# Kernel optimization log

Hardware: AMD Instinct MI355X
Metric: run time of the kernel (lower is better)

Reference implementation:

```python
import jax, jax.numpy as jnp
import numpy as np

N_EMBD = 2048
N_HEAD = 16
D_HEAD = N_EMBD // N_HEAD  # 128
B, T = 2, 2048
ROPE_BASE = 10000.0


def _rope_cos_sin(T, d, dtype):
    # (T, d) cos/sin tables, rotate-half convention
    inv_freq = 1.0 / (ROPE_BASE ** (jnp.arange(0, d, 2, dtype=jnp.float32) / d))
    ang = jnp.arange(T, dtype=jnp.float32)[:, None] * inv_freq[None, :]  # (T, d/2)
    cos = jnp.concatenate([jnp.cos(ang), jnp.cos(ang)], axis=-1).astype(dtype)
    sin = jnp.concatenate([jnp.sin(ang), jnp.sin(ang)], axis=-1).astype(dtype)
    return cos, sin


def _rotate_half(x):
    d = x.shape[-1] // 2
    return jnp.concatenate([-x[..., d:], x[..., :d]], axis=-1)


def setup_inputs() -> dict:
    key = jax.random.key(0)
    k1, k2, k3 = jax.random.split(key, 3)
    x = jax.random.normal(k1, (B, T, N_EMBD), dtype=jnp.float32)
    w_qkv = jax.random.normal(k2, (3 * N_EMBD, N_EMBD), dtype=jnp.float32) * 0.02
    w_proj = jax.random.normal(k3, (N_EMBD, N_EMBD), dtype=jnp.float32) * 0.02
    return {"x": x, "w_qkv": w_qkv, "w_proj": w_proj}


def reference(x, w_qkv, w_proj):
    Bq, Tq, C = x.shape
    H, D = N_HEAD, D_HEAD
    # fused QKV projection (torch Linear: x @ W.T)
    qkv = jnp.einsum('btc,fc->btf', x, w_qkv).reshape(Bq, Tq, 3, H, D)
    q, k, v = qkv[:, :, 0], qkv[:, :, 1], qkv[:, :, 2]  # (B,T,H,D)
    q = jnp.transpose(q, (0, 2, 1, 3))  # (B,H,T,D)
    k = jnp.transpose(k, (0, 2, 1, 3))
    v = jnp.transpose(v, (0, 2, 1, 3))
    # RoPE (start_pos = 0)
    cos, sin = _rope_cos_sin(Tq, D, x.dtype)  # (T,D)
    q = q * cos[None, None] + _rotate_half(q) * sin[None, None]
    k = k * cos[None, None] + _rotate_half(k) * sin[None, None]
    # causal SDPA
    scale = 1.0 / jnp.sqrt(jnp.asarray(D, x.dtype))
    scores = jnp.einsum('bhqd,bhkd->bhqk', q, k) * scale  # (B,H,T,T)
    causal = jnp.tril(jnp.ones((Tq, Tq), dtype=bool))
    scores = jnp.where(causal[None, None], scores, jnp.asarray(-jnp.inf, x.dtype))
    attn = jax.nn.softmax(scores, axis=-1)
    y = jnp.einsum('bhqk,bhkd->bhqd', attn, v)  # (B,H,T,D)
    y = jnp.transpose(y, (0, 2, 1, 3)).reshape(Bq, Tq, C)
    y = jnp.einsum('btc,fc->btf', y, w_proj)
    return y
```

## Files before the change

kernel.cpp:

```cpp
#include <hip/hip_runtime.h>
#include <hip/hip_bf16.h>
#include <math.h>

typedef __attribute__((ext_vector_type(8))) short short8;
typedef __attribute__((ext_vector_type(4))) short short4_t;
typedef __attribute__((ext_vector_type(4))) float f32x4;

#define Bb 2
#define Tt 2048
#define Hh 16
#define Dd 128
#define Cc 2048
#define Ff 6144

__device__ __forceinline__ size_t packed_idx(int row, int k) {
  return ((((size_t)(row >> 7) * 64 + (k >> 5)) * 8 + ((row >> 4) & 7)) * 512)
         + ((((k >> 3) & 3) * 16 + (row & 15)) * 8) + (k & 7);
}

__device__ __forceinline__ void gload_lds16(const void* g, void* l) {
  __builtin_amdgcn_global_load_lds(
      (const __attribute__((address_space(1))) void*)g,
      (__attribute__((address_space(3))) void*)l, 16, 0, 0);
}

__global__ __launch_bounds__(256) void pack_cast(
    const float* __restrict__ in, __hip_bfloat16* __restrict__ out, int n16)
{
  int t = blockIdx.x * 256 + threadIdx.x;
  if (t >= n16) return;
  int l = t & 63;
  int granule_lin = t >> 6;
  int g = granule_lin & 7;
  int slab = granule_lin >> 3;
  int ks = slab & 63;
  int m_tile = slab >> 6;
  int row = m_tile * 128 + g * 16 + (l & 15);
  int k = ks * 32 + (l >> 4) * 8;
  const float* src = in + (size_t)row * 2048 + k;
  float4 v0 = *(const float4*)src;
  float4 v1 = *(const float4*)(src + 4);
  __hip_bfloat16 tmp[8] = {
      __float2bfloat16(v0.x), __float2bfloat16(v0.y),
      __float2bfloat16(v0.z), __float2bfloat16(v0.w),
      __float2bfloat16(v1.x), __float2bfloat16(v1.y),
      __float2bfloat16(v1.z), __float2bfloat16(v1.w)};
  *(short8*)(out + (size_t)t * 8) = *(const short8*)tmp;
}

__device__ __forceinline__ void store_out(__hip_bfloat16* p, float v) { *p = __float2bfloat16(v); }
__device__ __forceinline__ void store_out(float* p, float v) { *p = v; }

template <typename OutT>
__global__ __launch_bounds__(512) void gemm_pk9(
    const __hip_bfloat16* __restrict__ Ap,
    const __hip_bfloat16* __restrict__ Bp,
    OutT* __restrict__ Cm, int N)
{
  __shared__ __align__(16) __hip_bfloat16 L[49152];
  const int tid  = threadIdx.x;
  const int wave = tid >> 6;
  const int lane = tid & 63;
  const int quad = lane >> 4;
  const int l16  = lane & 15;
  const int wm = wave >> 1;
  const int wn = wave & 1;
  const int bm = blockIdx.y * 256;
  const int bn = blockIdx.x * 128;
  const int NT = 32;
  const int ah = wm >> 1;
  const int ag = (wm & 1) * 4;

  const char* pA[2][2];
  const char* pB[2];
#pragma unroll
  for (int h = 0; h < 2; h++) {
#pragma unroll
    for (int c = 0; c < 2; c++) {
      int gi = wave * 2 + c;
      pA[h][c] = (const char*)Ap +
          ((size_t)(((bm >> 7) + h) * 64 + (gi >> 3)) * 8 + (gi & 7)) * 1024 + lane * 16;
    }
    pB[h] = (const char*)Bp +
        ((size_t)((bn >> 7) * 64 + h) * 8 + wave) * 1024 + lane * 16;
  }

#pragma unroll
  for (int h = 0; h < 2; h++) {
    gload_lds16(pA[h][0], &L[h * 12288 + (wave * 2 + 0) * 512]);
    gload_lds16(pA[h][1], &L[h * 12288 + (wave * 2 + 1) * 512]);
    gload_lds16(pB[h],    &L[h * 12288 + 8192 + wave * 512]);
    pA[h][0] += 16384; pA[h][1] += 16384; pB[h] += 16384;
  }

  f32x4 acc[4][4];
#pragma unroll
  for (int i = 0; i < 4; i++)
#pragma unroll
    for (int j = 0; j < 4; j++)
#pragma unroll
      for (int r = 0; r < 4; r++) acc[i][j][r] = 0.f;

#pragma unroll 1
  for (int t = 0; t < NT; ++t) {
    const int rs = (t & 1) * 2;
    const int ws = 2 - rs;
    const bool pre = (t + 1 < NT);

    if (pre) {
      gload_lds16(pA[0][0], &L[ws * 12288 + (wave * 2 + 0) * 512]);
      gload_lds16(pA[0][1], &L[ws * 12288 + (wave * 2 + 1) * 512]);
      gload_lds16(pB[0],    &L[ws * 12288 + 8192 + wave * 512]);
      __builtin_amdgcn_s_waitcnt(0xF73);
    } else {
      __builtin_amdgcn_s_waitcnt(0xF70);
    }
    __builtin_amdgcn_s_barrier();

    const __hip_bfloat16* A0 = &L[(rs + ah) * 12288];
    short8 bf[4][2];
#pragma unroll
    for (int j = 0; j < 4; j++)
#pragma unroll
      for (int k2 = 0; k2 < 2; k2++)
        bf[j][k2] = *(const short8*)(&L[(rs + k2) * 12288 + 8192 + (wn * 4 + j) * 512 + lane * 8]);
    {
      short8 af[2][2];
#pragma unroll
      for (int i = 0; i < 2; i++)
#pragma unroll
        for (int k2 = 0; k2 < 2; k2++)
          af[i][k2] = *(const short8*)(A0 + (k2 * 8 + ag + i) * 512 + lane * 8);
      __builtin_amdgcn_s_setprio(1);
#pragma unroll
      for (int i = 0; i < 2; i++)
#pragma unroll
        for (int j = 0; j < 4; j++)
#pragma unroll
          for (int k2 = 0; k2 < 2; k2++)
            acc[i][j] = __builtin_amdgcn_mfma_f32_16x16x32_bf16(
                af[i][k2], bf[j][k2], acc[i][j], 0, 0, 0);
      __builtin_amdgcn_s_setprio(0);
    }
    __builtin_amdgcn_s_barrier();

    if (pre) {
      gload_lds16(pA[1][0], &L[(ws + 1) * 12288 + (wave * 2 + 0) * 512]);
      gload_lds16(pA[1][1], &L[(ws + 1) * 12288 + (wave * 2 + 1) * 512]);
      gload_lds16(pB[1],    &L[(ws + 1) * 12288 + 8192 + wave * 512]);
    }
    {
      short8 af[2][2];
#pragma unroll
      for (int i = 0; i < 2; i++)
#pragma unroll
        for (int k2 = 0; k2 < 2; k2++)
          af[i][k2] = *(const short8*)(A0 + (k2 * 8 + ag + 2 + i) * 512 + lane * 8);
      __builtin_amdgcn_s_barrier();
      __builtin_amdgcn_s_setprio(1);
#pragma unroll
      for (int i = 0; i < 2; i++)
#pragma unroll
        for (int j = 0; j < 4; j++)
#pragma unroll
          for (int k2 = 0; k2 < 2; k2++)
            acc[2 + i][j] = __builtin_amdgcn_mfma_f32_16x16x32_bf16(
                af[i][k2], bf[j][k2], acc[2 + i][j], 0, 0, 0);
      __builtin_amdgcn_s_setprio(0);
    }
    __builtin_amdgcn_s_barrier();

    if (pre) {
#pragma unroll
      for (int h = 0; h < 2; h++) {
        pA[h][0] += 16384; pA[h][1] += 16384; pB[h] += 16384;
      }
    }
  }

#pragma unroll
  for (int i = 0; i < 4; i++)
#pragma unroll
    for (int j = 0; j < 4; j++)
#pragma unroll
      for (int r = 0; r < 4; r++) {
        int gm = bm + wm * 64 + i * 16 + quad * 4 + r;
        int gn = bn + wn * 64 + j * 16 + l16;
        store_out(Cm + (size_t)gm * N + gn, acc[i][j][r]);
      }
}

__global__ __launch_bounds__(256) void rope_qk(__hip_bfloat16* __restrict__ qkv)
{
  int tid = blockIdx.x * 256 + threadIdx.x;
  int d = tid & 63;
  int h = (tid >> 6) & 15;
  int t = (tid >> 10) & 2047;
  int bw = tid >> 21;
  int b = bw & 1, which = bw >> 1;
  size_t base = (size_t)(b * Tt + t) * Ff + which * 2048 + h * Dd + d;
  float inv = __expf(-(float)d * (9.210340371976184f / 64.0f));
  float ang = (float)t * inv;
  float c, s;
  __sincosf(ang, &s, &c);
  float x1 = __bfloat162float(qkv[base]);
  float x2 = __bfloat162float(qkv[base + 64]);
  float o1 = x1 * c - x2 * s;
  float o2 = x2 * c + x1 * s;
  if (which == 0) {
    o1 *= 0.08838834764831845f;
    o2 *= 0.08838834764831845f;
  }
  qkv[base]      = __float2bfloat16(o1);
  qkv[base + 64] = __float2bfloat16(o2);
}

__global__ __launch_bounds__(256) void transpose_v(
    const __hip_bfloat16* __restrict__ qkv, __hip_bfloat16* __restrict__ vt)
{
  __shared__ __hip_bfloat16 tile[64 * 65];
  int bh = blockIdx.y;
  int dt = blockIdx.x >> 5;
  int tt = blockIdx.x & 31;
  int b = bh >> 4, h = bh & 15;
  const __hip_bfloat16* src = qkv + (size_t)(b * Tt + tt * 64) * Ff + 4096 + h * Dd + dt * 64;
#pragma unroll
  for (int i = 0; i < 16; i++) {
    int lin = i * 256 + threadIdx.x;
    int tl = lin >> 6, dc = lin & 63;
    tile[tl * 65 + dc] = src[(size_t)tl * Ff + dc];
  }
  __syncthreads();
  __hip_bfloat16* dst = vt + ((size_t)bh * Dd + dt * 64) * Tt + tt * 64;
#pragma unroll
  for (int i = 0; i < 16; i++) {
    int lin = i * 256 + threadIdx.x;
    int dr = lin >> 6, tc = lin & 63;
    dst[(size_t)dr * Tt + tc] = tile[tc * 65 + dr];
  }
}

__global__ __launch_bounds__(512) void flash_attn5(
    const __hip_bfloat16* __restrict__ qkv,
    const __hip_bfloat16* __restrict__ vt,
    __hip_bfloat16* __restrict__ yat)
{
  __shared__ __align__(16) __hip_bfloat16 KsBuf[2][8192];
  __shared__ __align__(16) __hip_bfloat16 VsBuf[8192];
  __shared__ __align__(16) __hip_bfloat16 PsBuf[8 * 1088];
  const int tid  = threadIdx.x;
  const int wave = tid >> 6;
  const int lane = tid & 63;
  const int quad = lane >> 4;
  const int l16  = lane & 15;
  const int idx  = blockIdx.x;
  const int top  = idx >> 8;
  const int rest = idx & 255;
  const int p    = rest >> 5;
  const int bh   = rest & 31;
  const int qi   = top ? (15 - p) : p;
  const int b = bh >> 4, h = bh & 15;

  const char* kbase = (const char*)(qkv + (size_t)b * Tt * Ff + 2048 + h * Dd);
  const char* vbase = (const char*)(vt + (size_t)bh * Dd * Tt);
  __hip_bfloat16* Pw = PsBuf + wave * 1088;
  const int srow = lane & 15;
  const int scol = lane >> 4;

  const int qm0 = qi * 128;
  const int niter = 2 * qi + 2;

  short8 qf[4];
  {
    const __hip_bfloat16* qrow =
        qkv + (size_t)(b * Tt + qm0 + wave * 16 + l16) * Ff + h * Dd;
#pragma unroll
    for (int kc = 0; kc < 4; kc++)
      qf[kc] = *(const short8*)(qrow + kc * 32 + quad * 8);
  }

#pragma unroll
  for (int c = 0; c < 2; c++) {
    int chunk = wave * 2 + c;
    int j = chunk >> 2, kc = chunk & 3;
    const char* src = kbase + (size_t)(j * 16 + srow) * (Ff * 2) + kc * 64 + scol * 16;
    gload_lds16(src, KsBuf[0] + chunk * 512);
  }

  f32x4 oacc[8];
#pragma unroll
  for (int jd = 0; jd < 8; jd++)
#pragma unroll
    for (int r = 0; r < 4; r++) oacc[jd][r] = 0.f;
  float lsum[4];
#pragma unroll
  for (int r = 0; r < 4; r++) lsum[r] = 0.f;

#pragma unroll 1
  for (int kt = 0; kt < niter; ++kt) {
    __builtin_amdgcn_s_barrier();
#pragma unroll
    for (int c = 0; c < 2; c++) {
      int chunk = wave * 2 + c;
      int jd = chunk >> 1, k2 = chunk & 1;
      const char* src = vbase + (size_t)(jd * 16 + srow) * (Tt * 2) + kt * 128 + k2 * 64 + scol * 16;
      gload_lds16(src, VsBuf + chunk * 512);
    }
    if (kt + 1 < niter) {
#pragma unroll
      for (int c = 0; c < 2; c++) {
        int chunk = wave * 2 + c;
        int j = chunk >> 2, kc = chunk & 3;
        const char* src = kbase + (size_t)((kt + 1) * 64 + j * 16 + srow) * (Ff * 2) + kc * 64 + scol * 16;
        gload_lds16(src, KsBuf[(kt + 1) & 1] + chunk * 512);
      }
      __builtin_amdgcn_s_waitcnt(0xF74);
    } else {
      __builtin_amdgcn_s_waitcnt(0xF72);
    }
    __builtin_amdgcn_s_barrier();

    const __hip_bfloat16* KsB = KsBuf[kt & 1];
    const bool diag = (kt >= 2 * qi);

    f32x4 sacc[4];
#pragma unroll
    for (int j = 0; j < 4; j++)
#pragma unroll
      for (int r = 0; r < 4; r++) sacc[j][r] = 0.f;
#pragma unroll
    for (int j = 0; j < 4; j++)
#pragma unroll
      for (int kc = 0; kc < 4; kc++) {
        short8 kf = *(const short8*)(KsB + (j * 4 + kc) * 512 + lane * 8);
        sacc[j] = __builtin_amdgcn_mfma_f32_16x16x32_bf16(qf[kc], kf, sacc[j], 0, 0, 0);
      }

#pragma unroll
    for (int j = 0; j < 4; j++)
#pragma unroll
      for (int r = 0; r < 4; r++) {
        float v = sacc[j][r];
        if (diag) {
          int kg = kt * 64 + j * 16 + l16;
          int qg = qm0 + wave * 16 + quad * 4 + r;
          if (kg > qg) v = -INFINITY;
        }
        float p2 = __expf(v);
        lsum[r] += p2;
        Pw[(j * 2 + (l16 >> 3)) * 136 + (quad * 4 + r) * 8 + (l16 & 7)] = __float2bfloat16(p2);
      }

    if (kt + 1 < niter) {
      __builtin_amdgcn_s_waitcnt(0xF72);
    } else {
      __builtin_amdgcn_s_waitcnt(0xF70);
    }
    __builtin_amdgcn_s_barrier();

#pragma unroll
    for (int k2 = 0; k2 < 2; k2++) {
      short8 pf = *(const short8*)(Pw + (k2 * 4 + quad) * 136 + l16 * 8);
#pragma unroll
      for (int jd = 0; jd < 8; jd++) {
        short8 vf = *(const short8*)(VsBuf + (jd * 2 + k2) * 512 + lane * 8);
        oacc[jd] = __builtin_amdgcn_mfma_f32_16x16x32_bf16(pf, vf, oacc[jd], 0, 0, 0);
      }
    }
  }

#pragma unroll
  for (int off = 1; off < 16; off <<= 1)
#pragma unroll
    for (int r = 0; r < 4; r++)
      lsum[r] += __shfl_xor(lsum[r], off, 64);
  float linv[4];
#pragma unroll
  for (int r = 0; r < 4; r++) linv[r] = 1.f / lsum[r];
#pragma unroll
  for (int jd = 0; jd < 8; jd++)
#pragma unroll
    for (int r = 0; r < 4; r++) {
      int row = b * Tt + qm0 + wave * 16 + quad * 4 + r;
      int c = h * Dd + jd * 16 + l16;
      yat[packed_idx(row, c)] = __float2bfloat16(oacc[jd][r] * linv[r]);
    }
}

extern "C" void kernel_launch(void* const* d_in, const int* in_sizes, int n_in,
                              void* d_out, int out_size, void* d_ws, size_t ws_size,
                              hipStream_t stream) {
  (void)in_sizes; (void)n_in; (void)out_size; (void)ws_size;
  const float* x_f      = (const float*)d_in[0];
  const float* w_qkv_f  = (const float*)d_in[1];
  const float* w_proj_f = (const float*)d_in[2];
  float* out = (float*)d_out;

  char* ws = (char*)d_ws;
  __hip_bfloat16* qkv = (__hip_bfloat16*)ws;
  __hip_bfloat16* vt  = (__hip_bfloat16*)(ws + 50331648);
  __hip_bfloat16* yat = (__hip_bfloat16*)(ws + 67108864);
  __hip_bfloat16* xb  = (__hip_bfloat16*)(ws + 83886080);
  __hip_bfloat16* wqb = (__hip_bfloat16*)(ws + 100663296);
  __hip_bfloat16* wpb = (__hip_bfloat16*)(ws + 125829120);

  pack_cast<<<4096, 256, 0, stream>>>(x_f, xb, 1048576);
  pack_cast<<<6144, 256, 0, stream>>>(w_qkv_f, wqb, 1572864);
  pack_cast<<<2048, 256, 0, stream>>>(w_proj_f, wpb, 524288);

  gemm_pk9<__hip_bfloat16><<<dim3(48, 16), 512, 0, stream>>>(xb, wqb, qkv, 6144);
  rope_qk<<<32768, 256, 0, stream>>>(qkv);
  transpose_v<<<dim3(64, 32), 256, 0, stream>>>(qkv, vt);
  flash_attn5<<<512, 512, 0, stream>>>(qkv, vt, yat);
  gemm_pk9<float><<<dim3(16, 16), 512, 0, stream>>>(yat, wpb, out, 2048);
}
```

Baseline: 392.5 us.

## Remap GEMM blocks per XCD, regroup k-halves, and widen attention waves to 32 rows

The GEMM block index is remapped so that consecutive blocks on each XCD share the same column strip, which is meant to improve L2 reuse of B tiles. The GEMM inner loop now splits work by k-half across the two barriers instead of by row pair, so each phase loads 4 A and 4 B fragments. The flash-attention kernel moves from 8 waves of 16 query rows to 4 waves of 32 rows each. This reuses each K and V LDS fragment for two MFMAs and halves the thread count, at the cost of more registers per wave and each wave doing more loads.

After: 396.1 us. Within noise of the previous version (+0.9%).

```diff
diff --git a/kernel.cpp b/kernel.cpp
--- a/kernel.cpp
+++ b/kernel.cpp
@@ -65,8 +65,15 @@
   const int l16  = lane & 15;
   const int wm = wave >> 1;
   const int wn = wave & 1;
-  const int bm = blockIdx.y * 256;
-  const int bn = blockIdx.x * 128;
+  const int NBX = N >> 7;
+  const int cpx = NBX >> 3;
+  const int bid = blockIdx.y * NBX + blockIdx.x;
+  const int xcd = bid & 7;
+  const int pos = bid >> 3;
+  const int bx  = xcd * cpx + pos % cpx;
+  const int by  = pos / cpx;
+  const int bm = by * 256;
+  const int bn = bx * 128;
   const int NT = 32;
   const int ah = wm >> 1;
   const int ag = (wm & 1) * 4;
@@ -106,6 +113,7 @@
     const int rs = (t & 1) * 2;
     const int ws = 2 - rs;
     const bool pre = (t + 1 < NT);
+    const __hip_bfloat16* A0 = &L[(rs + ah) * 12288];
 
     if (pre) {
       gload_lds16(pA[0][0], &L[ws * 12288 + (wave * 2 + 0) * 512]);
@@ -116,30 +124,21 @@
       __builtin_amdgcn_s_waitcnt(0xF70);
     }
     __builtin_amdgcn_s_barrier();
-
-    const __hip_bfloat16* A0 = &L[(rs + ah) * 12288];
-    short8 bf[4][2];
-#pragma unroll
-    for (int j = 0; j < 4; j++)
-#pragma unroll
-      for (int k2 = 0; k2 < 2; k2++)
-        bf[j][k2] = *(const short8*)(&L[(rs + k2) * 12288 + 8192 + (wn * 4 + j) * 512 + lane * 8]);
     {
-      short8 af[2][2];
-#pragma unroll
-      for (int i = 0; i < 2; i++)
-#pragma unroll
-        for (int k2 = 0; k2 < 2; k2++)
-          af[i][k2] = *(const short8*)(A0 + (k2 * 8 + ag + i) * 512 + lane * 8);
+      short8 bf[4], af[4];
+#pragma unroll
+      for (int j = 0; j < 4; j++)
+        bf[j] = *(const short8*)(&L[rs * 12288 + 8192 + (wn * 4 + j) * 512 + lane * 8]);
+#pragma unroll
+      for (int i = 0; i < 4; i++)
+        af[i] = *(const short8*)(A0 + (ag + i) * 512 + lane * 8);
       __builtin_amdgcn_s_setprio(1);
 #pragma unroll
-      for (int i = 0; i < 2; i++)
+      for (int i = 0; i < 4; i++)
 #pragma unroll
         for (int j = 0; j < 4; j++)
-#pragma unroll
-          for (int k2 = 0; k2 < 2; k2++)
-            acc[i][j] = __builtin_amdgcn_mfma_f32_16x16x32_bf16(
-                af[i][k2], bf[j][k2], acc[i][j], 0, 0, 0);
+          acc[i][j] = __builtin_amdgcn_mfma_f32_16x16x32_bf16(
+              af[i], bf[j], acc[i][j], 0, 0, 0);
       __builtin_amdgcn_s_setprio(0);
     }
     __builtin_amdgcn_s_barrier();
@@ -150,22 +149,21 @@
       gload_lds16(pB[1],    &L[(ws + 1) * 12288 + 8192 + wave * 512]);
     }
     {
-      short8 af[2][2];
-#pragma unroll
-      for (int i = 0; i < 2; i++)
-#pragma unroll
-        for (int k2 = 0; k2 < 2; k2++)
-          af[i][k2] = *(const short8*)(A0 + (k2 * 8 + ag + 2 + i) * 512 + lane * 8);
+      short8 bf[4], af[4];
+#pragma unroll
+      for (int j = 0; j < 4; j++)
+        bf[j] = *(const short8*)(&L[(rs + 1) * 12288 + 8192 + (wn * 4 + j) * 512 + lane * 8]);
+#pragma unroll
+      for (int i = 0; i < 4; i++)
+        af[i] = *(const short8*)(A0 + (8 + ag + i) * 512 + lane * 8);
       __builtin_amdgcn_s_barrier();
       __builtin_amdgcn_s_setprio(1);
 #pragma unroll
-      for (int i = 0; i < 2; i++)
+      for (int i = 0; i < 4; i++)
 #pragma unroll
         for (int j = 0; j < 4; j++)
-#pragma unroll
-          for (int k2 = 0; k2 < 2; k2++)
-            acc[2 + i][j] = __builtin_amdgcn_mfma_f32_16x16x32_bf16(
-                af[i][k2], bf[j][k2], acc[2 + i][j], 0, 0, 0);
+          acc[i][j] = __builtin_amdgcn_mfma_f32_16x16x32_bf16(
+              af[i], bf[j], acc[i][j], 0, 0, 0);
       __builtin_amdgcn_s_setprio(0);
     }
     __builtin_amdgcn_s_barrier();
@@ -240,14 +238,14 @@
   }
 }
 
-__global__ __launch_bounds__(512) void flash_attn5(
+__global__ __launch_bounds__(256) void flash_attn6(
     const __hip_bfloat16* __restrict__ qkv,
     const __hip_bfloat16* __restrict__ vt,
     __hip_bfloat16* __restrict__ yat)
 {
   __shared__ __align__(16) __hip_bfloat16 KsBuf[2][8192];
   __shared__ __align__(16) __hip_bfloat16 VsBuf[8192];
-  __shared__ __align__(16) __hip_bfloat16 PsBuf[8 * 1088];
+  __shared__ __align__(16) __hip_bfloat16 PsBuf[4 * 2176];
   const int tid  = threadIdx.x;
   const int wave = tid >> 6;
   const int lane = tid & 63;
@@ -263,128 +261,143 @@
 
   const char* kbase = (const char*)(qkv + (size_t)b * Tt * Ff + 2048 + h * Dd);
   const char* vbase = (const char*)(vt + (size_t)bh * Dd * Tt);
-  __hip_bfloat16* Pw = PsBuf + wave * 1088;
+  __hip_bfloat16* Pw = PsBuf + wave * 2176;
   const int srow = lane & 15;
   const int scol = lane >> 4;
 
   const int qm0 = qi * 128;
   const int niter = 2 * qi + 2;
 
-  short8 qf[4];
-  {
+  short8 qf[2][4];
+#pragma unroll
+  for (int rg = 0; rg < 2; rg++) {
     const __hip_bfloat16* qrow =
-        qkv + (size_t)(b * Tt + qm0 + wave * 16 + l16) * Ff + h * Dd;
+        qkv + (size_t)(b * Tt + qm0 + wave * 32 + rg * 16 + l16) * Ff + h * Dd;
 #pragma unroll
     for (int kc = 0; kc < 4; kc++)
-      qf[kc] = *(const short8*)(qrow + kc * 32 + quad * 8);
-  }
-
-#pragma unroll
-  for (int c = 0; c < 2; c++) {
-    int chunk = wave * 2 + c;
+      qf[rg][kc] = *(const short8*)(qrow + kc * 32 + quad * 8);
+  }
+
+#pragma unroll
+  for (int c = 0; c < 4; c++) {
+    int chunk = wave * 4 + c;
     int j = chunk >> 2, kc = chunk & 3;
     const char* src = kbase + (size_t)(j * 16 + srow) * (Ff * 2) + kc * 64 + scol * 16;
     gload_lds16(src, KsBuf[0] + chunk * 512);
   }
 
-  f32x4 oacc[8];
-#pragma unroll
-  for (int jd = 0; jd < 8; jd++)
-#pragma unroll
-    for (int r = 0; r < 4; r++) oacc[jd][r] = 0.f;
-  float lsum[4];
-#pragma unroll
-  for (int r = 0; r < 4; r++) lsum[r] = 0.f;
+  f32x4 oacc[2][8];
+#pragma unroll
+  for (int rg = 0; rg < 2; rg++)
+#pragma unroll
+    for (int jd = 0; jd < 8; jd++)
+#pragma unroll
+      for (int r = 0; r < 4; r++) oacc[rg][jd][r] = 0.f;
+  float lsum[2][4];
+#pragma unroll
+  for (int rg = 0; rg < 2; rg++)
+#pragma unroll
+    for (int r = 0; r < 4; r++) lsum[rg][r] = 0.f;
 
 #pragma unroll 1
   for (int kt = 0; kt < niter; ++kt) {
     __builtin_amdgcn_s_barrier();
 #pragma unroll
-    for (int c = 0; c < 2; c++) {
-      int chunk = wave * 2 + c;
+    for (int c = 0; c < 4; c++) {
+      int chunk = wave * 4 + c;
       int jd = chunk >> 1, k2 = chunk & 1;
       const char* src = vbase + (size_t)(jd * 16 + srow) * (Tt * 2) + kt * 128 + k2 * 64 + scol * 16;
       gload_lds16(src, VsBuf + chunk * 512);
     }
     if (kt + 1 < niter) {
 #pragma unroll
-      for (int c = 0; c < 2; c++) {
-        int chunk = wave * 2 + c;
+      for (int c = 0; c < 4; c++) {
+        int chunk = wave * 4 + c;
         int j = chunk >> 2, kc = chunk & 3;
         const char* src = kbase + (size_t)((kt + 1) * 64 + j * 16 + srow) * (Ff * 2) + kc * 64 + scol * 16;
         gload_lds16(src, KsBuf[(kt + 1) & 1] + chunk * 512);
       }
+      __builtin_amdgcn_s_waitcnt(0xF78);
+    } else {
+      __builtin_amdgcn_s_waitcnt(0xF74);
+    }
+    __builtin_amdgcn_s_barrier();
+
+    const __hip_bfloat16* KsB = KsBuf[kt & 1];
+    const bool diag = (kt >= 2 * qi);
+
+    f32x4 s0[4], s1[4];
+#pragma unroll
+    for (int j = 0; j < 4; j++)
+#pragma unroll
+      for (int r = 0; r < 4; r++) { s0[j][r] = 0.f; s1[j][r] = 0.f; }
+#pragma unroll
+    for (int j = 0; j < 4; j++)
+#pragma unroll
+      for (int kc = 0; kc < 4; kc++) {
+        short8 kf = *(const short8*)(KsB + (j * 4 + kc) * 512 + lane * 8);
+        s0[j] = __builtin_amdgcn_mfma_f32_16x16x32_bf16(qf[0][kc], kf, s0[j], 0, 0, 0);
+        s1[j] = __builtin_amdgcn_mfma_f32_16x16x32_bf16(qf[1][kc], kf, s1[j], 0, 0, 0);
+      }
+
+#pragma unroll
+    for (int rg = 0; rg < 2; rg++) {
+#pragma unroll
+      for (int j = 0; j < 4; j++)
+#pragma unroll
+        for (int r = 0; r < 4; r++) {
+          float v = rg ? s1[j][r] : s0[j][r];
+          if (diag) {
+            int kg = kt * 64 + j * 16 + l16;
+            int qg = qm0 + wave * 32 + rg * 16 + quad * 4 + r;
+            if (kg > qg) v = -INFINITY;
+          }
+          float p2 = __expf(v);
+          lsum[rg][r] += p2;
+          Pw[rg * 1088 + (j * 2 + (l16 >> 3)) * 136 + (quad * 4 + r) * 8 + (l16 & 7)]
+              = __float2bfloat16(p2);
+        }
+    }
+
+    if (kt + 1 < niter) {
       __builtin_amdgcn_s_waitcnt(0xF74);
     } else {
-      __builtin_amdgcn_s_waitcnt(0xF72);
-    }
-    __builtin_amdgcn_s_barrier();
-
-    const __hip_bfloat16* KsB = KsBuf[kt & 1];
-    const bool diag = (kt >= 2 * qi);
-
-    f32x4 sacc[4];
-#pragma unroll
-    for (int j = 0; j < 4; j++)
-#pragma unroll
-      for (int r = 0; r < 4; r++) sacc[j][r] = 0.f;
-#pragma unroll
-    for (int j = 0; j < 4; j++)
-#pragma unroll
-      for (int kc = 0; kc < 4; kc++) {
-        short8 kf = *(const short8*)(KsB + (j * 4 + kc) * 512 + lane * 8);
-        sacc[j] = __builtin_amdgcn_mfma_f32_16x16x32_bf16(qf[kc], kf, sacc[j], 0, 0, 0);
-      }
-
-#pragma unroll
-    for (int j = 0; j < 4; j++)
-#pragma unroll
-      for (int r = 0; r < 4; r++) {
-        float v = sacc[j][r];
-        if (diag) {
-          int kg = kt * 64 + j * 16 + l16;
-          int qg = qm0 + wave * 16 + quad * 4 + r;
-          if (kg > qg) v = -INFINITY;
-        }
-        float p2 = __expf(v);
-        lsum[r] += p2;
-        Pw[(j * 2 + (l16 >> 3)) * 136 + (quad * 4 + r) * 8 + (l16 & 7)] = __float2bfloat16(p2);
-      }
-
-    if (kt + 1 < niter) {
-      __builtin_amdgcn_s_waitcnt(0xF72);
-    } else {
       __builtin_amdgcn_s_waitcnt(0xF70);
     }
     __builtin_amdgcn_s_barrier();
 
 #pragma unroll
     for (int k2 = 0; k2 < 2; k2++) {
-      short8 pf = *(const short8*)(Pw + (k2 * 4 + quad) * 136 + l16 * 8);
+      short8 pf0 = *(const short8*)(Pw + (k2 * 4 + quad) * 136 + l16 * 8);
+      short8 pf1 = *(const short8*)(Pw + 1088 + (k2 * 4 + quad) * 136 + l16 * 8);
 #pragma unroll
       for (int jd = 0; jd < 8; jd++) {
         short8 vf = *(const short8*)(VsBuf + (jd * 2 + k2) * 512 + lane * 8);
-        oacc[jd] = __builtin_amdgcn_mfma_f32_16x16x32_bf16(pf, vf, oacc[jd], 0, 0, 0);
-      }
-    }
-  }
-
-#pragma unroll
-  for (int off = 1; off < 16; off <<= 1)
-#pragma unroll
-    for (int r = 0; r < 4; r++)
-      lsum[r] += __shfl_xor(lsum[r], off, 64);
-  float linv[4];
-#pragma unroll
-  for (int r = 0; r < 4; r++) linv[r] = 1.f / lsum[r];
-#pragma unroll
-  for (int jd = 0; jd < 8; jd++)
-#pragma unroll
-    for (int r = 0; r < 4; r++) {
-      int row = b * Tt + qm0 + wave * 16 + quad * 4 + r;
-      int c = h * Dd + jd * 16 + l16;
-      yat[packed_idx(row, c)] = __float2bfloat16(oacc[jd][r] * linv[r]);
-    }
+        oacc[0][jd] = __builtin_amdgcn_mfma_f32_16x16x32_bf16(pf0, vf, oacc[0][jd], 0, 0, 0);
+        oacc[1][jd] = __builtin_amdgcn_mfma_f32_16x16x32_bf16(pf1, vf, oacc[1][jd], 0, 0, 0);
+      }
+    }
+  }
+
+#pragma unroll
+  for (int rg = 0; rg < 2; rg++) {
+#pragma unroll
+    for (int off = 1; off < 16; off <<= 1)
+#pragma unroll
+      for (int r = 0; r < 4; r++)
+        lsum[rg][r] += __shfl_xor(lsum[rg][r], off, 64);
+    float linv[4];
+#pragma unroll
+    for (int r = 0; r < 4; r++) linv[r] = 1.f / lsum[rg][r];
+#pragma unroll
+    for (int jd = 0; jd < 8; jd++)
+#pragma unroll
+      for (int r = 0; r < 4; r++) {
+        int row = b * Tt + qm0 + wave * 32 + rg * 16 + quad * 4 + r;
+        int c = h * Dd + jd * 16 + l16;
+        yat[packed_idx(row, c)] = __float2bfloat16(oacc[rg][jd][r] * linv[r]);
+      }
+  }
 }
 
 extern "C" void kernel_launch(void* const* d_in, const int* in_sizes, int n_in,
@@ -411,6 +424,6 @@
   gemm_pk9<__hip_bfloat16><<<dim3(48, 16), 512, 0, stream>>>(xb, wqb, qkv, 6144);
   rope_qk<<<32768, 256, 0, stream>>>(qkv);
   transpose_v<<<dim3(64, 32), 256, 0, stream>>>(qkv, vt);
-  flash_attn5<<<512, 512, 0, stream>>>(qkv, vt, yat);
+  flash_attn6<<<512, 256, 0, stream>>>(qkv, vt, yat);
   gemm_pk9<float><<<dim3(16, 16), 512, 0, stream>>>(yat, wpb, out, 2048);
 }
```

## Restructure GEMM into three-stage K pipeline with XCD-aware block remapping

Applied to the files above, without the earlier changes.

The GEMM kernel moves from two double-buffered half-tiles (48 KB LDS) to a ring of three 32-wide K stages (36 KB LDS). All loads for a stage are spread across waves, three per wave. Each wave now reads its A and B fragments fresh per stage, and the extra mid-iteration barrier is dropped. Block indices are also remapped so consecutive blocks on the same XCD share column tiles for better L2 reuse, and launch_bounds requests higher occupancy; the risks are more LDS fragment reads per MFMA and only one stage of prefetch slack.

New measurement: 395.3 us. Within noise of the previous version (+0.7%).

```diff
diff --git a/kernel.cpp b/kernel.cpp
--- a/kernel.cpp
+++ b/kernel.cpp
@@ -52,12 +52,12 @@
 __device__ __forceinline__ void store_out(float* p, float v) { *p = v; }
 
 template <typename OutT>
-__global__ __launch_bounds__(512) void gemm_pk9(
+__global__ __launch_bounds__(512, 4) void gemm_pk10(
     const __hip_bfloat16* __restrict__ Ap,
     const __hip_bfloat16* __restrict__ Bp,
     OutT* __restrict__ Cm, int N)
 {
-  __shared__ __align__(16) __hip_bfloat16 L[49152];
+  __shared__ __align__(16) __hip_bfloat16 L[3 * 12288];
   const int tid  = threadIdx.x;
   const int wave = tid >> 6;
   const int lane = tid & 63;
@@ -65,33 +65,42 @@
   const int l16  = lane & 15;
   const int wm = wave >> 1;
   const int wn = wave & 1;
-  const int bm = blockIdx.y * 256;
-  const int bn = blockIdx.x * 128;
+  const int NBX = N >> 7;
+  const int cpx = NBX >> 3;
+  const int bid = blockIdx.y * NBX + blockIdx.x;
+  const int xcd = bid & 7;
+  const int pos = bid >> 3;
+  const int bx  = xcd * cpx + pos % cpx;
+  const int by  = pos / cpx;
+  const int bm = by * 256;
+  const int bn = bx * 128;
   const int NT = 32;
-  const int ah = wm >> 1;
-  const int ag = (wm & 1) * 4;
-
-  const char* pA[2][2];
-  const char* pB[2];
-#pragma unroll
-  for (int h = 0; h < 2; h++) {
-#pragma unroll
-    for (int c = 0; c < 2; c++) {
-      int gi = wave * 2 + c;
-      pA[h][c] = (const char*)Ap +
-          ((size_t)(((bm >> 7) + h) * 64 + (gi >> 3)) * 8 + (gi & 7)) * 1024 + lane * 16;
-    }
-    pB[h] = (const char*)Bp +
-        ((size_t)((bn >> 7) * 64 + h) * 8 + wave) * 1024 + lane * 16;
-  }
-
-#pragma unroll
-  for (int h = 0; h < 2; h++) {
-    gload_lds16(pA[h][0], &L[h * 12288 + (wave * 2 + 0) * 512]);
-    gload_lds16(pA[h][1], &L[h * 12288 + (wave * 2 + 1) * 512]);
-    gload_lds16(pB[h],    &L[h * 12288 + 8192 + wave * 512]);
-    pA[h][0] += 16384; pA[h][1] += 16384; pB[h] += 16384;
-  }
+
+  const char* pg[3];
+  int ld[3];
+#pragma unroll
+  for (int c = 0; c < 3; c++) {
+    int gi = wave * 3 + c;
+    if (gi < 16) {
+      pg[c] = (const char*)Ap +
+          ((size_t)(((bm >> 7) + (gi >> 3)) * 64) * 8 + (gi & 7)) * 1024 + lane * 16;
+      ld[c] = gi * 512;
+    } else {
+      pg[c] = (const char*)Bp +
+          ((size_t)((bn >> 7) * 64) * 8 + (gi - 16)) * 1024 + lane * 16;
+      ld[c] = 8192 + (gi - 16) * 512;
+    }
+  }
+
+#define PK10_STAGE(ks)                                                         \
+  {                                                                            \
+    const int _s = (ks) % 3;                                                   \
+    _Pragma("unroll") for (int c = 0; c < 3; c++)                              \
+      gload_lds16(pg[c] + (size_t)(ks) * 8192, &L[_s * 12288 + ld[c]]);        \
+  }
+
+  PK10_STAGE(0);
+  PK10_STAGE(1);
 
   f32x4 acc[4][4];
 #pragma unroll
@@ -103,80 +112,59 @@
 
 #pragma unroll 1
   for (int t = 0; t < NT; ++t) {
-    const int rs = (t & 1) * 2;
-    const int ws = 2 - rs;
+    const int s0 = (2 * t) % 3;
+    const int s1 = (2 * t + 1) % 3;
     const bool pre = (t + 1 < NT);
 
     if (pre) {
-      gload_lds16(pA[0][0], &L[ws * 12288 + (wave * 2 + 0) * 512]);
-      gload_lds16(pA[0][1], &L[ws * 12288 + (wave * 2 + 1) * 512]);
-      gload_lds16(pB[0],    &L[ws * 12288 + 8192 + wave * 512]);
+      PK10_STAGE(2 * t + 2);
       __builtin_amdgcn_s_waitcnt(0xF73);
     } else {
       __builtin_amdgcn_s_waitcnt(0xF70);
     }
     __builtin_amdgcn_s_barrier();
-
-    const __hip_bfloat16* A0 = &L[(rs + ah) * 12288];
-    short8 bf[4][2];
-#pragma unroll
-    for (int j = 0; j < 4; j++)
-#pragma unroll
-      for (int k2 = 0; k2 < 2; k2++)
-        bf[j][k2] = *(const short8*)(&L[(rs + k2) * 12288 + 8192 + (wn * 4 + j) * 512 + lane * 8]);
     {
-      short8 af[2][2];
-#pragma unroll
-      for (int i = 0; i < 2; i++)
-#pragma unroll
-        for (int k2 = 0; k2 < 2; k2++)
-          af[i][k2] = *(const short8*)(A0 + (k2 * 8 + ag + i) * 512 + lane * 8);
+      short8 af[4], bf[4];
+#pragma unroll
+      for (int i = 0; i < 4; i++)
+        af[i] = *(const short8*)(&L[s0 * 12288 + (wm * 4 + i) * 512 + lane * 8]);
+#pragma unroll
+      for (int j = 0; j < 4; j++)
+        bf[j] = *(const short8*)(&L[s0 * 12288 + 8192 + (wn * 4 + j) * 512 + lane * 8]);
       __builtin_amdgcn_s_setprio(1);
 #pragma unroll
-      for (int i = 0; i < 2; i++)
+      for (int i = 0; i < 4; i++)
 #pragma unroll
         for (int j = 0; j < 4; j++)
-#pragma unroll
-          for (int k2 = 0; k2 < 2; k2++)
-            acc[i][j] = __builtin_amdgcn_mfma_f32_16x16x32_bf16(
-                af[i][k2], bf[j][k2], acc[i][j], 0, 0, 0);
+          acc[i][j] = __builtin_amdgcn_mfma_f32_16x16x32_bf16(
+              af[i], bf[j], acc[i][j], 0, 0, 0);
       __builtin_amdgcn_s_setprio(0);
     }
     __builtin_amdgcn_s_barrier();
 
     if (pre) {
-      gload_lds16(pA[1][0], &L[(ws + 1) * 12288 + (wave * 2 + 0) * 512]);
-      gload_lds16(pA[1][1], &L[(ws + 1) * 12288 + (wave * 2 + 1) * 512]);
-      gload_lds16(pB[1],    &L[(ws + 1) * 12288 + 8192 + wave * 512]);
+      PK10_STAGE(2 * t + 3);
     }
     {
-      short8 af[2][2];
-#pragma unroll
-      for (int i = 0; i < 2; i++)
-#pragma unroll
-        for (int k2 = 0; k2 < 2; k2++)
-          af[i][k2] = *(const short8*)(A0 + (k2 * 8 + ag + 2 + i) * 512 + lane * 8);
-      __builtin_amdgcn_s_barrier();
+      short8 af[4], bf[4];
+#pragma unroll
+      for (int i = 0; i < 4; i++)
+        af[i] = *(const short8*)(&L[s1 * 12288 + (wm * 4 + i) * 512 + lane * 8]);
+#pragma unroll
+      for (int j = 0; j < 4; j++)
+        bf[j] = *(const short8*)(&L[s1 * 12288 + 8192 + (wn * 4 + j) * 512 + lane * 8]);
       __builtin_amdgcn_s_setprio(1);
 #pragma unroll
-      for (int i = 0; i < 2; i++)
+      for (int i = 0; i < 4; i++)
 #pragma unroll
         for (int j = 0; j < 4; j++)
-#pragma unroll
-          for (int k2 = 0; k2 < 2; k2++)
-            acc[2 + i][j] = __builtin_amdgcn_mfma_f32_16x16x32_bf16(
-                af[i][k2], bf[j][k2], acc[2 + i][j], 0, 0, 0);
+          acc[i][j] = __builtin_amdgcn_mfma_f32_16x16x32_bf16(
+              af[i], bf[j], acc[i][j], 0, 0, 0);
       __builtin_amdgcn_s_setprio(0);
     }
     __builtin_amdgcn_s_barrier();
-
-    if (pre) {
-#pragma unroll
-      for (int h = 0; h < 2; h++) {
-        pA[h][0] += 16384; pA[h][1] += 16384; pB[h] += 16384;
-      }
-    }
-  }
+  }
+#undef PK10_STAGE
 
 #pragma unroll
   for (int i = 0; i < 4; i++)
@@ -408,9 +396,9 @@
   pack_cast<<<6144, 256, 0, stream>>>(w_qkv_f, wqb, 1572864);
   pack_cast<<<2048, 256, 0, stream>>>(w_proj_f, wpb, 524288);
 
-  gemm_pk9<__hip_bfloat16><<<dim3(48, 16), 512, 0, stream>>>(xb, wqb, qkv, 6144);
+  gemm_pk10<__hip_bfloat16><<<dim3(48, 16), 512, 0, stream>>>(xb, wqb, qkv, 6144);
   rope_qk<<<32768, 256, 0, stream>>>(qkv);
   transpose_v<<<dim3(64, 32), 256, 0, stream>>>(qkv, vt);
   flash_attn5<<<512, 512, 0, stream>>>(qkv, vt, yat);
-  gemm_pk9<float><<<dim3(16, 16), 512, 0, stream>>>(yat, wpb, out, 2048);
-}
+  gemm_pk10<float><<<dim3(16, 16), 512, 0, stream>>>(yat, wpb, out, 2048);
+}
```
